# Performance work log

Hardware: AMD Instinct MI355X
Metric: run time of the kernel (lower is better)

## Reference

```python
import jax, jax.numpy as jnp
import numpy as np

B, M, D, P, T = 512, 16, 128, 16, 4096
GAMMA = 1.0  # similarity_size


def setup_inputs() -> dict:
    key = jax.random.key(0)
    k1, k2, k3, k4, k5 = jax.random.split(key, 5)
    phi = jax.random.normal(k1, (B, P), dtype=jnp.float32)
    state = jax.random.normal(k2, (B, D), dtype=jnp.float32)
    trajectories = jax.random.normal(k3, (T, D), dtype=jnp.float32)
    # Stand-in per-model KAARMA state-transition parameters (linear recurrent + input map, tanh)
    A = jax.random.normal(k4, (M, D, D), dtype=jnp.float32) * (1.0 / np.sqrt(D))
    B_in = jax.random.normal(k5, (M, P, D), dtype=jnp.float32) * (1.0 / np.sqrt(P))
    return {"phi": phi, "state": state, "trajectories": trajectories, "A": A, "B_in": B_in}


def reference(phi, state, trajectories, A, B_in):
    # per-model state update: new_state[b,m,:] = tanh(state @ A_m + phi @ B_m)
    new_state = jnp.tanh(
        jnp.einsum("bd,mdh->bmh", state, A) + jnp.einsum("bp,mph->bmh", phi, B_in)
    )  # [B, M, D]
    # RBF similarity vs trajectory set via ||s||^2 + ||t||^2 - 2 s.t (single batched GEMM)
    s_sq = jnp.sum(new_state * new_state, axis=-1, keepdims=True)      # [B, M, 1]
    t_sq = jnp.sum(trajectories * trajectories, axis=-1)               # [T]
    cross = jnp.einsum("bmd,td->bmt", new_state, trajectories)         # [B, M, T]
    sq_dist = jnp.maximum(s_sq + t_sq[None, None, :] - 2.0 * cross, 0.0)
    sim = jnp.exp(-GAMMA * sq_dist)                                    # [B, M, T]
    output = sim.reshape(phi.shape[0], -1)                             # [B, M*T]
    return output, new_state
```

## Files before the change

### kernel.cpp

```cpp
#include <hip/hip_runtime.h>
#include <hip/hip_bf16.h>
#include <cstdint>
#include <cstddef>

#define NB 512
#define NM 16
#define ND 128
#define NP 16
#define NT 4096

typedef __bf16 bf16x8 __attribute__((ext_vector_type(8)));
typedef float f32x4 __attribute__((ext_vector_type(4)));

static_assert(sizeof(bf16x8) == 16, "bf16x8 must be 16B");

__device__ __forceinline__ void gload_lds16(const void* g, void* l) {
  __builtin_amdgcn_global_load_lds(
      (const __attribute__((address_space(1))) unsigned int*)g,
      (__attribute__((address_space(3))) unsigned int*)l, 16, 0, 0);
}

__global__ __launch_bounds__(256) void prep_kernel(
    const float* __restrict__ phi, const float* __restrict__ state,
    const float* __restrict__ traj, const float* __restrict__ A,
    const float* __restrict__ Bin, float* __restrict__ ns_out,
    __bf16* __restrict__ ns_bf, __bf16* __restrict__ tj_bf,
    float* __restrict__ s_sq, float* __restrict__ t_sq) {
  __shared__ alignas(16) float sSt[16 * 128];
  __shared__ alignas(16) float sPhi[16 * 16];
  __shared__ alignas(16) float sRes[16 * 128];
  const int tid = threadIdx.x;
  const int bx = blockIdx.x;

  if (bx < 512) {
    const int m = bx & 15;
    const int b0 = (bx >> 4) * 16;
    const float4* S4 = (const float4*)(state + (size_t)b0 * 128);
    float4* sSt4 = (float4*)sSt;
    sSt4[tid] = S4[tid];
    sSt4[tid + 256] = S4[tid + 256];
    sPhi[tid] = phi[b0 * 16 + tid];
    __syncthreads();

    const int h2 = tid & 63;
    const int rgrp = tid >> 6;
    const float* Ap = A + (size_t)m * 16384 + h2;
    const float* Bp = Bin + (size_t)m * 2048 + h2;

    float acc[2][4];
#pragma unroll
    for (int hi = 0; hi < 2; ++hi)
#pragma unroll
      for (int j = 0; j < 4; ++j) acc[hi][j] = 0.f;

#pragma unroll 4
    for (int c = 0; c < 32; ++c) {
      float a0[4], a1[4];
#pragma unroll
      for (int u = 0; u < 4; ++u) {
        a0[u] = Ap[(size_t)(c * 4 + u) * 128];
        a1[u] = Ap[(size_t)(c * 4 + u) * 128 + 64];
      }
#pragma unroll
      for (int j = 0; j < 4; ++j) {
        const f32x4 sv = *(const f32x4*)&sSt[(rgrp * 4 + j) * 128 + c * 4];
#pragma unroll
        for (int u = 0; u < 4; ++u) {
          acc[0][j] = fmaf(sv[u], a0[u], acc[0][j]);
          acc[1][j] = fmaf(sv[u], a1[u], acc[1][j]);
        }
      }
    }
#pragma unroll
    for (int pc = 0; pc < 4; ++pc) {
      float b0v[4], b1v[4];
#pragma unroll
      for (int u = 0; u < 4; ++u) {
        b0v[u] = Bp[(size_t)(pc * 4 + u) * 128];
        b1v[u] = Bp[(size_t)(pc * 4 + u) * 128 + 64];
      }
#pragma unroll
      for (int j = 0; j < 4; ++j) {
        const f32x4 pv = *(const f32x4*)&sPhi[(rgrp * 4 + j) * 16 + pc * 4];
#pragma unroll
        for (int u = 0; u < 4; ++u) {
          acc[0][j] = fmaf(pv[u], b0v[u], acc[0][j]);
          acc[1][j] = fmaf(pv[u], b1v[u], acc[1][j]);
        }
      }
    }

#pragma unroll
    for (int j = 0; j < 4; ++j) {
      const int row = rgrp * 4 + j;
      const int R = (b0 + row) * 16 + m;
      const float v0 = tanhf(acc[0][j]);
      const float v1 = tanhf(acc[1][j]);
      ns_out[(size_t)R * 128 + h2] = v0;
      ns_out[(size_t)R * 128 + h2 + 64] = v1;
      sRes[row * 128 + h2] = v0;
      sRes[row * 128 + h2 + 64] = v1;
      float s = v0 * v0 + v1 * v1;
#pragma unroll
      for (int o = 32; o > 0; o >>= 1) s += __shfl_xor(s, o);
      if (h2 == 0) s_sq[R] = s;
    }
    __syncthreads();

    {
      const int row = tid >> 4;
      const int kb = tid & 15;
      const f32x4 r0 = *(const f32x4*)&sRes[row * 128 + kb * 8];
      const f32x4 r1 = *(const f32x4*)&sRes[row * 128 + kb * 8 + 4];
      bf16x8 o;
#pragma unroll
      for (int i = 0; i < 4; ++i) {
        o[i] = (__bf16)r0[i];
        o[i + 4] = (__bf16)r1[i];
      }
      const int R = (b0 + row) * 16 + m;
      *(bf16x8*)(ns_bf + (size_t)R * 128 + ((kb ^ m) * 8)) = o;
    }
  } else {
    const int t0 = (bx - 512) * 128;
    const int t = t0 + (tid >> 1);
    const int half = tid & 1;
    float s = 0.f;
#pragma unroll
    for (int q = 0; q < 8; ++q) {
      const int kb = half * 8 + q;
      const f32x4 v0 = *(const f32x4*)&traj[(size_t)t * 128 + kb * 8];
      const f32x4 v1 = *(const f32x4*)&traj[(size_t)t * 128 + kb * 8 + 4];
      s += v0[0] * v0[0] + v0[1] * v0[1] + v0[2] * v0[2] + v0[3] * v0[3];
      s += v1[0] * v1[0] + v1[1] * v1[1] + v1[2] * v1[2] + v1[3] * v1[3];
      bf16x8 o;
#pragma unroll
      for (int i = 0; i < 4; ++i) {
        o[i] = (__bf16)v0[i];
        o[i + 4] = (__bf16)v1[i];
      }
      *(bf16x8*)(tj_bf + (size_t)t * 128 + ((kb ^ (t & 15)) * 8)) = o;
    }
    s += __shfl_xor(s, 1);
    if (half == 0) t_sq[t] = s;
  }
}

__global__ __launch_bounds__(256) void sim_kernel(
    const __bf16* __restrict__ ns_bf, const __bf16* __restrict__ tj_bf,
    const float* __restrict__ s_sq, const float* __restrict__ t_sq,
    float* __restrict__ out) {
  __shared__ alignas(16) __bf16 sA[64 * 128];
  __shared__ alignas(16) __bf16 sB[128 * 128];
  __shared__ float sSq[64];
  __shared__ float sTq[128];
  const int tid = threadIdx.x;
  const int lane = tid & 63;
  const int w = tid >> 6;
  const int R0 = blockIdx.x * 64;
  const int C0 = blockIdx.y * 128;

  const char* gA = (const char*)(ns_bf + (size_t)R0 * 128);
  const char* gB = (const char*)(tj_bf + (size_t)C0 * 128);
#pragma unroll
  for (int it = 0; it < 4; ++it) {
    const int off = w * 4096 + it * 1024;
    gload_lds16(gA + off + lane * 16, (char*)sA + off);
  }
#pragma unroll
  for (int it = 0; it < 8; ++it) {
    const int off = w * 8192 + it * 1024;
    gload_lds16(gB + off + lane * 16, (char*)sB + off);
  }
  if (tid < 64)
    sSq[tid] = s_sq[R0 + tid];
  else if (tid < 192)
    sTq[tid - 64] = t_sq[C0 + tid - 64];
  __syncthreads();

  const int abase = (w >> 1) * 32;
  const int cbase = (w & 1) * 64;
  const int l15 = lane & 15;
  const int quad = lane >> 4;

  f32x4 acc[2][4];
#pragma unroll
  for (int i = 0; i < 2; ++i)
#pragma unroll
    for (int j = 0; j < 4; ++j) acc[i][j] = (f32x4){0.f, 0.f, 0.f, 0.f};

#pragma unroll
  for (int ks = 0; ks < 4; ++ks) {
    const int kb = quad + ks * 4;
    const int koff = (kb ^ l15) * 8;
    bf16x8 af[2], bfr[4];
#pragma unroll
    for (int i = 0; i < 2; ++i)
      af[i] = *(const bf16x8*)&sA[(abase + i * 16 + l15) * 128 + koff];
#pragma unroll
    for (int i = 0; i < 4; ++i)
      bfr[i] = *(const bf16x8*)&sB[(cbase + i * 16 + l15) * 128 + koff];
#pragma unroll
    for (int ri = 0; ri < 2; ++ri)
#pragma unroll
      for (int ci = 0; ci < 4; ++ci)
        acc[ri][ci] = __builtin_amdgcn_mfma_f32_16x16x32_bf16(
            bfr[ci], af[ri], acc[ri][ci], 0, 0, 0);
  }

#pragma unroll
  for (int ri = 0; ri < 2; ++ri) {
    const int nsrow = abase + ri * 16 + l15;
    const float sq = sSq[nsrow];
    float* orow = out + (size_t)(R0 + nsrow) * NT + C0;
#pragma unroll
    for (int ci = 0; ci < 4; ++ci) {
      const int t4 = cbase + ci * 16 + quad * 4;
      const f32x4 tq = *(const f32x4*)&sTq[t4];
      f32x4 r;
#pragma unroll
      for (int k = 0; k < 4; ++k) {
        const float d = fmaxf(sq + tq[k] - 2.f * acc[ri][ci][k], 0.f);
        r[k] = __expf(-d);
      }
      *(f32x4*)&orow[t4] = r;
    }
  }
}

extern "C" void kernel_launch(void* const* d_in, const int* in_sizes, int n_in,
                              void* d_out, int out_size, void* d_ws,
                              size_t ws_size, hipStream_t stream) {
  (void)in_sizes; (void)n_in; (void)out_size; (void)ws_size;
  const float* phi   = (const float*)d_in[0];
  const float* state = (const float*)d_in[1];
  const float* traj  = (const float*)d_in[2];
  const float* A     = (const float*)d_in[3];
  const float* Bin   = (const float*)d_in[4];

  float* out = (float*)d_out;
  float* out_ns = out + (size_t)NB * NM * NT;

  char* ws = (char*)d_ws;
  __bf16* ns_bf = (__bf16*)ws;
  __bf16* tj_bf = (__bf16*)(ws + (2u << 20));
  float* s_sq   = (float*)(ws + (3u << 20));
  float* t_sq   = (float*)(ws + (3u << 20) + (32u << 10));

  prep_kernel<<<544, 256, 0, stream>>>(phi, state, traj, A, Bin, out_ns, ns_bf,
                                       tj_bf, s_sq, t_sq);
  dim3 g2(NB * NM / 64, NT / 128);
  sim_kernel<<<g2, 256, 0, stream>>>(ns_bf, tj_bf, s_sq, t_sq, out);
}
```

Baseline: 173.6 us.

## Enlarge sim tiles and double-buffer trajectory tiles across column steps

The similarity kernel now computes a 128x256 output tile per block instead of 64x128. The A tile stays resident in LDS while four 64-column trajectory sub-tiles are streamed through a double buffer with asynchronous global-to-LDS loads, prefetching the next sub-tile while the current one goes through MFMA and the exp epilogue. This cuts redundant reloads of the state and trajectory tiles and overlaps load latency with compute. In exchange there are four times fewer blocks, twice the LDS per block and extra barriers, which may reduce occupancy for a kernel dominated by output stores.

```diff
diff --git a/kernel.cpp b/kernel.cpp
--- a/kernel.cpp
+++ b/kernel.cpp
@@ -150,81 +150,96 @@
     const __bf16* __restrict__ ns_bf, const __bf16* __restrict__ tj_bf,
     const float* __restrict__ s_sq, const float* __restrict__ t_sq,
     float* __restrict__ out) {
-  __shared__ alignas(16) __bf16 sA[64 * 128];
-  __shared__ alignas(16) __bf16 sB[128 * 128];
-  __shared__ float sSq[64];
-  __shared__ float sTq[128];
+  __shared__ alignas(16) __bf16 sA[128 * 128];
+  __shared__ alignas(16) __bf16 sB[2][64 * 128];
+  __shared__ float sSq[128];
+  __shared__ float sTq[256];
   const int tid = threadIdx.x;
   const int lane = tid & 63;
   const int w = tid >> 6;
-  const int R0 = blockIdx.x * 64;
-  const int C0 = blockIdx.y * 128;
+  const int R0 = blockIdx.x * 128;
+  const int Cg = blockIdx.y * 256;
 
   const char* gA = (const char*)(ns_bf + (size_t)R0 * 128);
-  const char* gB = (const char*)(tj_bf + (size_t)C0 * 128);
+  const char* gB = (const char*)(tj_bf + (size_t)Cg * 128);
+
+#pragma unroll
+  for (int it = 0; it < 8; ++it) {
+    const int off = w * 8192 + it * 1024;
+    gload_lds16(gA + off + lane * 16, (char*)sA + off);
+  }
 #pragma unroll
   for (int it = 0; it < 4; ++it) {
     const int off = w * 4096 + it * 1024;
-    gload_lds16(gA + off + lane * 16, (char*)sA + off);
-  }
-#pragma unroll
-  for (int it = 0; it < 8; ++it) {
-    const int off = w * 8192 + it * 1024;
-    gload_lds16(gB + off + lane * 16, (char*)sB + off);
-  }
-  if (tid < 64)
+    gload_lds16(gB + off + lane * 16, (char*)sB[0] + off);
+  }
+  if (tid < 128)
     sSq[tid] = s_sq[R0 + tid];
-  else if (tid < 192)
-    sTq[tid - 64] = t_sq[C0 + tid - 64];
-  __syncthreads();
-
-  const int abase = (w >> 1) * 32;
-  const int cbase = (w & 1) * 64;
+  sTq[tid] = t_sq[Cg + tid];
+
+  const int abase = w * 32;
   const int l15 = lane & 15;
   const int quad = lane >> 4;
 
-  f32x4 acc[2][4];
-#pragma unroll
-  for (int i = 0; i < 2; ++i)
-#pragma unroll
-    for (int j = 0; j < 4; ++j) acc[i][j] = (f32x4){0.f, 0.f, 0.f, 0.f};
-
-#pragma unroll
-  for (int ks = 0; ks < 4; ++ks) {
-    const int kb = quad + ks * 4;
-    const int koff = (kb ^ l15) * 8;
-    bf16x8 af[2], bfr[4];
+  __syncthreads();
+
+#pragma unroll
+  for (int j = 0; j < 4; ++j) {
+    const int cur = j & 1;
+    if (j < 3) {
+#pragma unroll
+      for (int it = 0; it < 4; ++it) {
+        const int off = w * 4096 + it * 1024;
+        gload_lds16(gB + (size_t)(j + 1) * 16384 + off + lane * 16,
+                    (char*)sB[1 - cur] + off);
+      }
+    }
+
+    f32x4 acc[2][4];
 #pragma unroll
     for (int i = 0; i < 2; ++i)
-      af[i] = *(const bf16x8*)&sA[(abase + i * 16 + l15) * 128 + koff];
-#pragma unroll
-    for (int i = 0; i < 4; ++i)
-      bfr[i] = *(const bf16x8*)&sB[(cbase + i * 16 + l15) * 128 + koff];
-#pragma unroll
-    for (int ri = 0; ri < 2; ++ri)
-#pragma unroll
-      for (int ci = 0; ci < 4; ++ci)
-        acc[ri][ci] = __builtin_amdgcn_mfma_f32_16x16x32_bf16(
-            bfr[ci], af[ri], acc[ri][ci], 0, 0, 0);
-  }
-
-#pragma unroll
-  for (int ri = 0; ri < 2; ++ri) {
-    const int nsrow = abase + ri * 16 + l15;
-    const float sq = sSq[nsrow];
-    float* orow = out + (size_t)(R0 + nsrow) * NT + C0;
-#pragma unroll
-    for (int ci = 0; ci < 4; ++ci) {
-      const int t4 = cbase + ci * 16 + quad * 4;
-      const f32x4 tq = *(const f32x4*)&sTq[t4];
-      f32x4 r;
-#pragma unroll
-      for (int k = 0; k < 4; ++k) {
-        const float d = fmaxf(sq + tq[k] - 2.f * acc[ri][ci][k], 0.f);
-        r[k] = __expf(-d);
-      }
-      *(f32x4*)&orow[t4] = r;
-    }
+#pragma unroll
+      for (int c = 0; c < 4; ++c) acc[i][c] = (f32x4){0.f, 0.f, 0.f, 0.f};
+
+#pragma unroll
+    for (int ks = 0; ks < 4; ++ks) {
+      const int kb = quad + ks * 4;
+      const int koff = (kb ^ l15) * 8;
+      bf16x8 af[2], bfr[4];
+#pragma unroll
+      for (int i = 0; i < 2; ++i)
+        af[i] = *(const bf16x8*)&sA[(abase + i * 16 + l15) * 128 + koff];
+#pragma unroll
+      for (int c = 0; c < 4; ++c)
+        bfr[c] = *(const bf16x8*)&sB[cur][(c * 16 + l15) * 128 + koff];
+#pragma unroll
+      for (int ri = 0; ri < 2; ++ri)
+#pragma unroll
+        for (int ci = 0; ci < 4; ++ci)
+          acc[ri][ci] = __builtin_amdgcn_mfma_f32_16x16x32_bf16(
+              bfr[ci], af[ri], acc[ri][ci], 0, 0, 0);
+    }
+
+#pragma unroll
+    for (int ri = 0; ri < 2; ++ri) {
+      const int nsrow = abase + ri * 16 + l15;
+      const float sq = sSq[nsrow];
+      float* orow = out + (size_t)(R0 + nsrow) * NT + Cg + j * 64;
+#pragma unroll
+      for (int ci = 0; ci < 4; ++ci) {
+        const int t4 = ci * 16 + quad * 4;
+        const f32x4 tq = *(const f32x4*)&sTq[j * 64 + t4];
+        f32x4 r;
+#pragma unroll
+        for (int k = 0; k < 4; ++k) {
+          const float d = fmaxf(sq + tq[k] - 2.f * acc[ri][ci][k], 0.f);
+          r[k] = __expf(-d);
+        }
+        *(f32x4*)&orow[t4] = r;
+      }
+    }
+
+    if (j < 3) __syncthreads();
   }
 }
 
@@ -249,6 +264,6 @@
 
   prep_kernel<<<544, 256, 0, stream>>>(phi, state, traj, A, Bin, out_ns, ns_bf,
                                        tj_bf, s_sq, t_sq);
-  dim3 g2(NB * NM / 64, NT / 128);
+  dim3 g2(NB * NM / 128, NT / 256);
   sim_kernel<<<g2, 256, 0, stream>>>(ns_bf, tj_bf, s_sq, t_sq, out);
 }
```

Result: faster. 170.0 us (-2.1%).
